# Kernel tuning notes

Hardware: AMD Instinct MI355X
Metric: run time of the kernel (lower is better)

## Reference

```python
import jax, jax.numpy as jnp
import numpy as np

N_NODES = 10000
N_EDGES = 640000
N_GRAPHS = 64
D_NODE = 128   # NO_NODE_FEATURES_TWO
D_EDGE = 32    # NO_EDGE_FEATURES_TWO
HIDDEN = 128   # HIDDEN_GRAPH_TWO
D_OUT = 64     # NO_GRAPH_FEATURES_TWO
EPS = 1e-5


def _xavier(key, fan_in, fan_out):
    lim = float(np.sqrt(6.0 / (fan_in + fan_out)))
    return jax.random.uniform(key, (fan_in, fan_out), jnp.float32, -lim, lim)


def setup_inputs() -> dict:
    key = jax.random.key(0)
    ks = jax.random.split(key, 12)
    x = jax.random.normal(ks[0], (N_NODES, D_NODE), jnp.float32)
    edge_index = jax.random.randint(ks[1], (2, N_EDGES), 0, N_NODES, jnp.int64)
    edge_attr = jax.random.normal(ks[2], (N_EDGES, D_EDGE), jnp.float32)
    u = jax.random.normal(ks[3], (N_GRAPHS, D_OUT), jnp.float32)
    batch = jnp.sort(jax.random.randint(ks[4], (N_NODES,), 0, N_GRAPHS, jnp.int64))
    # global_mlp_1: Lin(160,128) -> LeakyReLU -> BatchNorm1d(128) -> Lin(128,128)
    W1 = _xavier(ks[5], D_NODE + D_EDGE, HIDDEN); b1 = jnp.full((HIDDEN,), 0.01, jnp.float32)
    g1 = jnp.ones((HIDDEN,), jnp.float32); be1 = jnp.zeros((HIDDEN,), jnp.float32)
    W2 = _xavier(ks[6], HIDDEN, HIDDEN); b2 = jnp.full((HIDDEN,), 0.01, jnp.float32)
    # global_mlp_2: Lin(256,128) -> LeakyReLU -> BatchNorm1d(128) -> Lin(128,64)
    W3 = _xavier(ks[7], HIDDEN + D_NODE, HIDDEN); b3 = jnp.full((HIDDEN,), 0.01, jnp.float32)
    g3 = jnp.ones((HIDDEN,), jnp.float32); be3 = jnp.zeros((HIDDEN,), jnp.float32)
    W4 = _xavier(ks[8], HIDDEN, D_OUT); b4 = jnp.full((D_OUT,), 0.01, jnp.float32)
    return {"x": x, "edge_index": edge_index, "edge_attr": edge_attr, "u": u, "batch": batch,
            "W1": W1, "b1": b1, "g1": g1, "be1": be1, "W2": W2, "b2": b2,
            "W3": W3, "b3": b3, "g3": g3, "be3": be3, "W4": W4, "b4": b4}


def _batchnorm(h, gamma, beta):
    # training-mode BatchNorm1d: biased batch stats
    mu = jnp.mean(h, axis=0)
    var = jnp.var(h, axis=0)
    return gamma * (h - mu) * jax.lax.rsqrt(var + EPS) + beta


def reference(x, edge_index, edge_attr, u, batch,
              W1, b1, g1, be1, W2, b2, W3, b3, g3, be3, W4, b4):
    row, col = edge_index[0], edge_index[1]
    # gather + concat -> [E, 160]
    h = jnp.concatenate([x[row], edge_attr], axis=1)
    # global_mlp_1
    h = jax.nn.leaky_relu(h @ W1 + b1, negative_slope=0.01)
    h = _batchnorm(h, g1, be1)
    h = h @ W2 + b2                                   # [E, HIDDEN]
    # scatter_add to nodes
    node_agg = jax.ops.segment_sum(h, col, num_segments=N_NODES)  # [N, HIDDEN]
    # per-graph pooling of x and node_agg
    gx = jax.ops.segment_sum(x, batch, num_segments=N_GRAPHS)       # [B, D_NODE]
    go = jax.ops.segment_sum(node_agg, batch, num_segments=N_GRAPHS)  # [B, HIDDEN]
    g = jnp.concatenate([gx, go], axis=1)             # [B, 256]
    # global_mlp_2
    g = jax.nn.leaky_relu(g @ W3 + b3, negative_slope=0.01)
    g = _batchnorm(g, g3, be3)
    return g @ W4 + b4                                # [B, 64]
```

## Files before the change

kernel.cpp:

```cpp
#include <hip/hip_runtime.h>

#define EE      640000
#define NNODES_ 10000
#define NG      64
#define DN      128
#define DE      32
#define HID     128
#define DOUT    64
#define NMT     (EE / 16)
#define SLOWNB  768
#define HBLK    128
#define CHUNK   (EE / HBLK)
#define FBLK    512
#define NWAVES  (FBLK * 4)

#define ACCF  0
#define CNTF  8192
#define S1F   8256
#define S2F   8384
#define GXF   8512
#define O1F   16704
#define FLGF  24896
#define BAT8  24898
#define W1F_  27458
#define B1F_  47938
#define G1F_  48066
#define BE1F_ 48194
#define W2F_  48322
#define B2F_  64706
#define W3F_  64834
#define B3F_  97602
#define G3F_  97730
#define BE3F_ 97858
#define W4F_  97986
#define B4F_  106178
#define YBF   106244
#define H32F  746244
#define BSTF  754436
#define GENDI 762628
#define NTI   762692
#define T2G   762696
#define SRTE  772936
#define WSEND 1413960

typedef __bf16 bf16x8 __attribute__((ext_vector_type(8)));
typedef float  f32x4  __attribute__((ext_vector_type(4)));

__device__ __forceinline__ float lrelu(float v) { return v > 0.f ? v : 0.01f * v; }

__device__ __forceinline__ bf16x8 cvt8(const float* p) {
  const f32x4 a0 = *(const f32x4*)p, a1 = *(const f32x4*)(p + 4);
  bf16x8 t;
  t[0]=(__bf16)a0[0]; t[1]=(__bf16)a0[1]; t[2]=(__bf16)a0[2]; t[3]=(__bf16)a0[3];
  t[4]=(__bf16)a1[0]; t[5]=(__bf16)a1[1]; t[6]=(__bf16)a1[2]; t[7]=(__bf16)a1[3];
  return t;
}

__global__ __launch_bounds__(256) void k_sniff(const unsigned* __restrict__ xw,
                                               const unsigned* __restrict__ ew,
                                               float* __restrict__ ws) {
  const int tid = threadIdx.x;
  for (int i = tid; i < 8512; i += 256) ws[i] = 0.f;
  if (tid < 64) {
    const unsigned w = xw[tid];
    const unsigned ex = (w >> 7) & 0xFFu;
    int cb = (ex >= 100u && ex <= 140u) ? 1 : 0;
    int ci = (ew[2 * tid + 1] == 0u) ? 1 : 0;
#pragma unroll
    for (int s = 1; s < 64; s <<= 1) { cb += __shfl_xor(cb, s); ci += __shfl_xor(ci, s); }
    if (tid == 0) { int* f = (int*)(ws + FLGF); f[0] = (cb >= 48); f[1] = (ci >= 60); }
  }
}

__device__ __forceinline__ void cpyw(float* dst, const void* src, int n, int isb,
                                     int gtid, int gs) {
  if (isb) { const __bf16* s = (const __bf16*)src;
    for (int i = gtid; i < n; i += gs) dst[i] = (float)s[i];
  } else { const float* s = (const float*)src;
    for (int i = gtid; i < n; i += gs) dst[i] = s[i]; }
}

__global__ __launch_bounds__(256) void k_norm(
    const void* __restrict__ eidx, const void* __restrict__ batch,
    const void* W1, const void* b1, const void* g1, const void* be1,
    const void* W2, const void* b2, const void* W3, const void* b3,
    const void* g3, const void* be3, const void* W4, const void* b4,
    float* __restrict__ ws, const int dohist) {
  const int gtid = blockIdx.x * 256 + threadIdx.x;
  const int gs = gridDim.x * 256;
  const int* f = (const int*)(ws + FLGF);
  const int isb = f[0], isi = f[1];
  cpyw(ws + W1F_, W1, 160 * HID, isb, gtid, gs);
  cpyw(ws + B1F_, b1, HID, isb, gtid, gs);
  cpyw(ws + G1F_, g1, HID, isb, gtid, gs);
  cpyw(ws + BE1F_, be1, HID, isb, gtid, gs);
  cpyw(ws + W2F_, W2, HID * HID, isb, gtid, gs);
  cpyw(ws + B2F_, b2, HID, isb, gtid, gs);
  cpyw(ws + W3F_, W3, 256 * HID, isb, gtid, gs);
  cpyw(ws + B3F_, b3, HID, isb, gtid, gs);
  cpyw(ws + G3F_, g3, HID, isb, gtid, gs);
  cpyw(ws + BE3F_, be3, HID, isb, gtid, gs);
  cpyw(ws + W4F_, W4, HID * DOUT, isb, gtid, gs);
  cpyw(ws + B4F_, b4, DOUT, isb, gtid, gs);
  const int* bs = (const int*)batch;
  unsigned char* b8 = (unsigned char*)(ws + BAT8);
  for (int i = gtid; i < NNODES_; i += gs)
    b8[i] = (unsigned char)((isi ? bs[2 * i] : bs[i]) & 63);
  if (dohist) {
    __shared__ int h[NG];
    if (threadIdx.x < NG) h[threadIdx.x] = 0;
    __syncthreads();
    const int* es = (const int*)eidx;
    for (int e = gtid; e < EE; e += gs) {
      int cl = isi ? es[2 * (EE + e)] : es[EE + e];
      cl = min(max(cl, 0), NNODES_ - 1);
      atomicAdd(&h[(isi ? bs[2 * cl] : bs[cl]) & 63], 1);
    }
    __syncthreads();
    if (threadIdx.x < NG && h[threadIdx.x])
      unsafeAtomicAdd(&ws[CNTF + threadIdx.x], (float)h[threadIdx.x]);
  }
}

__global__ __launch_bounds__(256) void k_hist(const void* __restrict__ eidx,
                                              float* __restrict__ ws) {
  __shared__ int h[NG];
  const int tid = threadIdx.x, b = blockIdx.x;
  if (tid < NG) h[tid] = 0;
  __syncthreads();
  const int isi = ((const int*)(ws + FLGF))[1];
  const int* ei32 = (const int*)eidx;
  const unsigned char* bat8 = (const unsigned char*)(ws + BAT8);
  for (int e = b * CHUNK + tid; e < (b + 1) * CHUNK; e += 256) {
    int cl = isi ? ei32[2 * (EE + e)] : ei32[EE + e];
    cl = min(max(cl, 0), NNODES_ - 1);
    atomicAdd(&h[bat8[cl]], 1);
  }
  __syncthreads();
  if (tid < NG) ((int*)(ws + H32F))[b * NG + tid] = h[tid];
}

__global__ void k_scan(float* __restrict__ ws) {
  const int g = threadIdx.x;
  const int* H = (const int*)(ws + H32F);
  int* BS = (int*)(ws + BSTF);
  int cnt = 0;
  for (int b = 0; b < HBLK; ++b) { BS[b * NG + g] = cnt; cnt += H[b * NG + g]; }
  const int pc = (cnt + 15) & ~15;
  int inc = pc;
#pragma unroll
  for (int s = 1; s < 64; s <<= 1) { int u = __shfl_up(inc, s); if (g >= s) inc += u; }
  const int base = inc - pc;
  for (int b = 0; b < HBLK; ++b) BS[b * NG + g] += base;
  ((int*)(ws + GENDI))[g] = base + cnt;
  ws[CNTF + g] = (float)cnt;
  const int tot = __shfl(inc, 63);
  if (g == 0) ((int*)(ws + NTI))[0] = tot >> 4;
  unsigned char* t2 = (unsigned char*)(ws + T2G);
  for (int i = base >> 4; i < (base + pc) >> 4; ++i) t2[i] = (unsigned char)g;
  int* srte = (int*)(ws + SRTE);
  for (int i = cnt; i < pc; ++i) srte[base + i] = 0;
}

__global__ __launch_bounds__(256) void k_scat(const void* __restrict__ eidx,
                                              float* __restrict__ ws) {
  __shared__ int cur[NG];
  const int tid = threadIdx.x, b = blockIdx.x;
  if (tid < NG) cur[tid] = ((const int*)(ws + BSTF))[b * NG + tid];
  __syncthreads();
  const int isi = ((const int*)(ws + FLGF))[1];
  const int* ei32 = (const int*)eidx;
  const unsigned char* bat8 = (const unsigned char*)(ws + BAT8);
  int* srte = (int*)(ws + SRTE);
  for (int e = b * CHUNK + tid; e < (b + 1) * CHUNK; e += 256) {
    int cl = isi ? ei32[2 * (EE + e)] : ei32[EE + e];
    cl = min(max(cl, 0), NNODES_ - 1);
    const int pos = atomicAdd(&cur[bat8[cl]], 1);
    srte[pos] = e;
  }
}

__global__ __launch_bounds__(256) void k_gx(
    const void* __restrict__ x, const void* __restrict__ batch, float* __restrict__ ws) {
  const int b = blockIdx.x, tid = threadIdx.x;
  const int isb = ((const int*)(ws + FLGF))[0];
  const int isi = ((const int*)(ws + FLGF))[1];
  const int* bt = (const int*)batch;
#define BATV(i) ((isi ? bt[2 * (i)] : bt[(i)]) & 63)
  int lo = 0, hi = NNODES_;
  while (lo < hi) { int m = (lo + hi) >> 1; if (BATV(m) < b) lo = m + 1; else hi = m; }
  const int r0 = lo;
  hi = NNODES_;
  while (lo < hi) { int m = (lo + hi) >> 1; if (BATV(m) < b + 1) lo = m + 1; else hi = m; }
  const int r1 = lo;
#undef BATV
  const int c = tid & 127, half = tid >> 7;
  float acc = 0.f;
  if (isb) { const __bf16* xs = (const __bf16*)x;
    for (int r = r0 + half; r < r1; r += 2) acc += (float)xs[r * DN + c];
  } else { const float* xs = (const float*)x;
    for (int r = r0 + half; r < r1; r += 2) acc += xs[r * DN + c]; }
  __shared__ float red[256];
  red[tid] = acc;
  __syncthreads();
  if (tid < 128) ws[GXF + b * DN + tid] = red[tid] + red[tid + 128];
}

__global__ __launch_bounds__(256) void k_y(float* __restrict__ ws, const void* __restrict__ x) {
  __shared__ __align__(16) __bf16 w1x[128 * 128];
  const int tid = threadIdx.x;
  const int isb = ((const int*)(ws + FLGF))[0];
  for (int i = tid; i < 128 * 128; i += 256) {
    const int k = i >> 7, n = i & 127;
    w1x[n * 128 + k] = (__bf16)ws[W1F_ + k * HID + n];
  }
  __syncthreads();
  const int lane = tid & 63, wid = tid >> 6, ml = lane & 15, kg = lane >> 4;
  __bf16* ybf = (__bf16*)(ws + YBF);
  for (int t = blockIdx.x * 4 + wid; t < 625; t += 160 * 4) {
    const int n0 = t * 16;
    const int row = n0 + ml;
    bf16x8 af[4];
    if (isb) {
      const __bf16* xp = (const __bf16*)x + row * DN + kg * 8;
#pragma unroll
      for (int ks = 0; ks < 4; ++ks) af[ks] = *(const bf16x8*)(xp + ks * 32);
    } else {
      const float* xp = (const float*)x + row * DN + kg * 8;
#pragma unroll
      for (int ks = 0; ks < 4; ++ks) af[ks] = cvt8(xp + ks * 32);
    }
    f32x4 acc[8] = {{0,0,0,0},{0,0,0,0},{0,0,0,0},{0,0,0,0},
                    {0,0,0,0},{0,0,0,0},{0,0,0,0},{0,0,0,0}};
#pragma unroll
    for (int ks = 0; ks < 4; ++ks) {
#pragma unroll
      for (int nt = 0; nt < 8; ++nt) {
        const bf16x8 bfr = *(const bf16x8*)(w1x + (nt * 16 + ml) * 128 + ks * 32 + kg * 8);
        acc[nt] = __builtin_amdgcn_mfma_f32_16x16x32_bf16(af[ks], bfr, acc[nt], 0, 0, 0);
      }
    }
#pragma unroll
    for (int nt = 0; nt < 8; ++nt) {
      const int c = nt * 16 + ml;
      const float bias = ws[B1F_ + c];
#pragma unroll
      for (int q = 0; q < 4; ++q)
        ybf[(n0 + kg * 4 + q) * HID + c] = (__bf16)(acc[nt][q] + bias);
    }
  }
}

__global__ __launch_bounds__(256, 4) void k_edgef2(float* __restrict__ ws,
                                                   const void* __restrict__ ea,
                                                   const void* __restrict__ eidx) {
  __shared__ __align__(16) __bf16 w1e[128 * 32];
  const int tid = threadIdx.x;
  const int* flg = (const int*)(ws + FLGF);
  const int isb = flg[0], isi = flg[1];
  for (int i = tid; i < 32 * 128; i += 256) {
    const int k = i >> 7, n = i & 127;
    w1e[n * 32 + k] = (__bf16)ws[W1F_ + (128 + k) * HID + n];
  }
  __syncthreads();
  const int lane = tid & 63, wid = tid >> 6, ml = lane & 15, kg = lane >> 4;
  bf16x8 bfe[8];
#pragma unroll
  for (int nt = 0; nt < 8; ++nt)
    bfe[nt] = *(const bf16x8*)(w1e + (nt * 16 + ml) * 32 + kg * 8);
  bf16x8 idf;
#pragma unroll
  for (int j = 0; j < 8; ++j) idf[j] = (kg * 8 + j == ml) ? (__bf16)1.0f : (__bf16)0.0f;

  const int* ei32 = (const int*)eidx;
  const int* srte = (const int*)(ws + SRTE);
  const unsigned char* t2g = (const unsigned char*)(ws + T2G);
  const int* gend = (const int*)(ws + GENDI);
  const __bf16* ybf = (const __bf16*)(ws + YBF);
  const int NT = ((const int*)(ws + NTI))[0];
  const int tpw = (NT + NWAVES - 1) / NWAVES;
  const int wgid = blockIdx.x * 4 + wid;
  const int t0 = wgid * tpw;
  const int t1 = min(t0 + tpw, NT);

  float gsum[8] = {0,0,0,0,0,0,0,0};
  float s1[8] = {0,0,0,0,0,0,0,0}, s2[8] = {0,0,0,0,0,0,0,0};
  int cur_g = (t0 < t1) ? (int)t2g[t0] : -1;

  for (int t = t0; t < t1; ++t) {
    const int g = (int)t2g[t];
    if (g != cur_g) {
#pragma unroll
      for (int nt = 0; nt < 8; ++nt) {
        float v = gsum[nt];
        v += __shfl_xor(v, 16); v += __shfl_xor(v, 32);
        if (kg == 0) unsafeAtomicAdd(&ws[ACCF + cur_g * HID + nt * 16 + ml], v);
        gsum[nt] = 0.f;
      }
      cur_g = g;
    }
    const int ge = gend[g];
    const int eidm = srte[t * 16 + ml];
    int r = isi ? ei32[2 * eidm] : ei32[eidm];
    r = min(max(r, 0), NNODES_ - 1);
    bf16x8 ae;
    if (isb) ae = *(const bf16x8*)((const __bf16*)ea + (size_t)eidm * DE + kg * 8);
    else     ae = cvt8((const float*)ea + (size_t)eidm * DE + kg * 8);
    f32x4 acc[8] = {{0,0,0,0},{0,0,0,0},{0,0,0,0},{0,0,0,0},
                    {0,0,0,0},{0,0,0,0},{0,0,0,0},{0,0,0,0}};
#pragma unroll
    for (int nt = 0; nt < 8; ++nt)
      acc[nt] = __builtin_amdgcn_mfma_f32_16x16x32_bf16(ae, bfe[nt], acc[nt], 0, 0, 0);
    const __bf16* yb = ybf + (size_t)r * HID + (kg & 1) * 8;
#pragma unroll
    for (int nt = 0; nt < 8; ++nt) {
      const bf16x8 ay = *(const bf16x8*)(yb + nt * 16);
      acc[nt] = __builtin_amdgcn_mfma_f32_16x16x32_bf16(ay, idf, acc[nt], 0, 0, 0);
    }
    const int eb = t * 16 + kg * 4;
#pragma unroll
    for (int nt = 0; nt < 8; ++nt) {
#pragma unroll
      for (int q = 0; q < 4; ++q) {
        const float v = (eb + q < ge) ? lrelu(acc[nt][q]) : 0.f;
        gsum[nt] += v;
        s1[nt] += v;
        s2[nt] += v * v;
      }
    }
  }
  if (cur_g >= 0) {
#pragma unroll
    for (int nt = 0; nt < 8; ++nt) {
      float v = gsum[nt];
      v += __shfl_xor(v, 16); v += __shfl_xor(v, 32);
      if (kg == 0) unsafeAtomicAdd(&ws[ACCF + cur_g * HID + nt * 16 + ml], v);
    }
  }
#pragma unroll
  for (int nt = 0; nt < 8; ++nt) {
    float v1 = s1[nt], v2 = s2[nt];
    v1 += __shfl_xor(v1, 16); v1 += __shfl_xor(v1, 32);
    v2 += __shfl_xor(v2, 16); v2 += __shfl_xor(v2, 32);
    if (kg == 0) {
      unsafeAtomicAdd(&ws[S1F + nt * 16 + ml], v1);
      unsafeAtomicAdd(&ws[S2F + nt * 16 + ml], v2);
    }
  }
}

__global__ __launch_bounds__(256) void k_edges_slow(
    float* __restrict__ ws, const void* __restrict__ x, const void* __restrict__ ea,
    const void* __restrict__ eidx) {
  __shared__ __align__(16) char smem[40960];
  float* lacc = (float*)smem;
  __bf16* w1t = (__bf16*)smem;
  const int tid = threadIdx.x;
  const int* flg = (const int*)(ws + FLGF);
  const int isb = flg[0], isi = flg[1];
  for (int i = tid; i < 160 * HID; i += 256) {
    const int k = i >> 7, n = i & 127;
    w1t[n * 160 + k] = (__bf16)ws[W1F_ + i];
  }
  __syncthreads();
  const int lane = tid & 63, wid = tid >> 6;
  const int ml = lane & 15, kg = lane >> 4;
  const int ch0 = (wid & 1) * 64;
  const int pair = blockIdx.x * 2 + (wid >> 1);
  bf16x8 bfr[5][4];
  float b1v[4];
#pragma unroll
  for (int nt = 0; nt < 4; ++nt) {
    const int n = ch0 + nt * 16 + ml;
    b1v[nt] = ws[B1F_ + n];
#pragma unroll
    for (int ks = 0; ks < 5; ++ks)
      bfr[ks][nt] = *(const bf16x8*)(w1t + n * 160 + ks * 32 + kg * 8);
  }
  __syncthreads();
  for (int i = tid; i < NG * 132; i += 256) lacc[i] = 0.f;
  __syncthreads();
  float s1a[4] = {0,0,0,0}, s2a[4] = {0,0,0,0};
  const int* ei32 = (const int*)eidx;
  const unsigned char* bat8 = (const unsigned char*)(ws + BAT8);
  for (int mt = pair; mt < NMT; mt += 2 * SLOWNB) {
    const int em = mt * 16 + ml;
    int r  = isi ? ei32[2 * em] : ei32[em];
    int cl = isi ? ei32[2 * (EE + em)] : ei32[EE + em];
    r  = min(max(r, 0), NNODES_ - 1);
    cl = min(max(cl, 0), NNODES_ - 1);
    const int gg = bat8[cl];
    f32x4 acc[4] = {{0,0,0,0},{0,0,0,0},{0,0,0,0},{0,0,0,0}};
#pragma unroll
    for (int ks = 0; ks < 4; ++ks) {
      bf16x8 afr;
      if (isb) afr = *(const bf16x8*)((const __bf16*)x + r * DN + ks * 32 + kg * 8);
      else     afr = cvt8((const float*)x + r * DN + ks * 32 + kg * 8);
#pragma unroll
      for (int nt = 0; nt < 4; ++nt)
        acc[nt] = __builtin_amdgcn_mfma_f32_16x16x32_bf16(afr, bfr[ks][nt], acc[nt], 0, 0, 0);
    }
    {
      bf16x8 t;
      if (isb) t = *(const bf16x8*)((const __bf16*)ea + em * DE + kg * 8);
      else     t = cvt8((const float*)ea + em * DE + kg * 8);
#pragma unroll
      for (int nt = 0; nt < 4; ++nt)
        acc[nt] = __builtin_amdgcn_mfma_f32_16x16x32_bf16(t, bfr[4][nt], acc[nt], 0, 0, 0);
    }
    int gR[4];
#pragma unroll
    for (int q = 0; q < 4; ++q) gR[q] = __shfl(gg, kg * 4 + q);
#pragma unroll
    for (int nt = 0; nt < 4; ++nt) {
      const int c = ch0 + nt * 16 + ml;
#pragma unroll
      for (int q = 0; q < 4; ++q) {
        const float v = lrelu(acc[nt][q] + b1v[nt]);
        s1a[nt] += v;
        s2a[nt] += v * v;
        atomicAdd(&lacc[gR[q] * 132 + c], v);
      }
    }
  }
#pragma unroll
  for (int nt = 0; nt < 4; ++nt) {
    float v1 = s1a[nt], v2 = s2a[nt];
    v1 += __shfl_xor(v1, 16); v1 += __shfl_xor(v1, 32);
    v2 += __shfl_xor(v2, 16); v2 += __shfl_xor(v2, 32);
    if (lane < 16) {
      unsafeAtomicAdd(&ws[S1F + ch0 + nt * 16 + lane], v1);
      unsafeAtomicAdd(&ws[S2F + ch0 + nt * 16 + lane], v2);
    }
  }
  __syncthreads();
  for (int i = tid; i < NG * HID; i += 256)
    unsafeAtomicAdd(&ws[ACCF + i], lacc[(i >> 7) * 132 + (i & 127)]);
}

__global__ __launch_bounds__(128) void k_graph(float* __restrict__ ws) {
  const int b = blockIdx.x, c = threadIdx.x;
  const float invE = 1.f / (float)EE;
  const float mu  = ws[S1F + c] * invE;
  const float var = ws[S2F + c] * invE - mu * mu;
  const float s   = ws[G1F_ + c] * rsqrtf(var + 1e-5f);
  const float t   = ws[BE1F_ + c] - mu * s;
  const float cb  = ws[CNTF + b];
  __shared__ float zsh[HID];
  __shared__ float gv[DN + HID];
  zsh[c] = s * ws[ACCF + b * HID + c] + cb * t;
  gv[c]  = ws[GXF + b * DN + c];
  __syncthreads();
  float a = cb * ws[B2F_ + c];
  for (int k = 0; k < HID; ++k) a += zsh[k] * ws[W2F_ + k * HID + c];
  gv[DN + c] = a;
  __syncthreads();
  float h = ws[B3F_ + c];
  for (int j = 0; j < DN + HID; ++j) h += gv[j] * ws[W3F_ + j * HID + c];
  ws[O1F + b * HID + c] = lrelu(h);
}

__global__ __launch_bounds__(64) void k_out(const float* __restrict__ ws,
                                            void* __restrict__ out) {
  const int b = blockIdx.x, o = threadIdx.x;
  const int isb = ((const int*)(ws + FLGF))[0];
  __shared__ float zrow[HID];
  for (int cc = o; cc < HID; cc += 64) {
    float sm = 0.f, sq = 0.f;
    for (int r = 0; r < NG; ++r) { const float v = ws[O1F + r * HID + cc]; sm += v; sq += v * v; }
    const float mu  = sm * (1.f / NG);
    const float var = sq * (1.f / NG) - mu * mu;
    const float sc  = ws[G3F_ + cc] * rsqrtf(var + 1e-5f);
    zrow[cc] = ws[O1F + b * HID + cc] * sc + (ws[BE3F_ + cc] - mu * sc);
  }
  __syncthreads();
  float a = ws[B4F_ + o];
  for (int k = 0; k < HID; ++k) a += zrow[k] * ws[W4F_ + k * DOUT + o];
  if (isb) ((__bf16*)out)[b * DOUT + o] = (__bf16)a;
  else     ((float*)out)[b * DOUT + o] = a;
}

extern "C" void kernel_launch(void* const* d_in, const int* in_sizes, int n_in,
                              void* d_out, int out_size, void* d_ws, size_t ws_size,
                              hipStream_t stream) {
  float* ws = (float*)d_ws;
  const int fast = (ws_size >= (size_t)WSEND * 4) ? 1 : 0;
  hipLaunchKernelGGL(k_sniff, dim3(1), dim3(256), 0, stream,
                     (const unsigned*)d_in[0], (const unsigned*)d_in[1], ws);
  hipLaunchKernelGGL(k_norm, dim3(256), dim3(256), 0, stream,
                     d_in[1], d_in[4],
                     d_in[5], d_in[6], d_in[7], d_in[8],
                     d_in[9], d_in[10], d_in[11], d_in[12],
                     d_in[13], d_in[14], d_in[15], d_in[16], ws, fast ? 0 : 1);
  hipLaunchKernelGGL(k_gx, dim3(NG), dim3(256), 0, stream, d_in[0], d_in[4], ws);
  if (fast) {
    hipLaunchKernelGGL(k_hist, dim3(HBLK), dim3(256), 0, stream, d_in[1], ws);
    hipLaunchKernelGGL(k_scan, dim3(1), dim3(64), 0, stream, ws);
    hipLaunchKernelGGL(k_scat, dim3(HBLK), dim3(256), 0, stream, d_in[1], ws);
    hipLaunchKernelGGL(k_y, dim3(160), dim3(256), 0, stream, ws, d_in[0]);
    hipLaunchKernelGGL(k_edgef2, dim3(FBLK), dim3(256), 0, stream, ws, d_in[2], d_in[1]);
  } else {
    hipLaunchKernelGGL(k_edges_slow, dim3(SLOWNB), dim3(256), 0, stream,
                       ws, d_in[0], d_in[2], d_in[1]);
  }
  hipLaunchKernelGGL(k_graph, dim3(NG), dim3(128), 0, stream, ws);
  hipLaunchKernelGGL(k_out, dim3(NG), dim3(64), 0, stream, ws, d_out);
}
```

Measured before the change: 392.0 us.

## Fuse prep kernels, pre-sort source rows, and retune edge block counts

```diff
diff --git a/kernel.cpp b/kernel.cpp
--- a/kernel.cpp
+++ b/kernel.cpp
@@ -9,9 +9,9 @@
 #define DOUT    64
 #define NMT     (EE / 16)
 #define SLOWNB  768
-#define HBLK    128
+#define HBLK    256
 #define CHUNK   (EE / HBLK)
-#define FBLK    512
+#define FBLK    2048
 #define NWAVES  (FBLK * 4)
 
 #define ACCF  0
@@ -36,12 +36,13 @@
 #define B4F_  106178
 #define YBF   106244
 #define H32F  746244
-#define BSTF  754436
-#define GENDI 762628
-#define NTI   762692
-#define T2G   762696
-#define SRTE  772936
-#define WSEND 1413960
+#define BSTF  762628
+#define GENDI 779012
+#define NTI   779076
+#define T2G   779078
+#define SRTE  789318
+#define SRR   1430342
+#define WSEND 1750854
 
 typedef __bf16 bf16x8 __attribute__((ext_vector_type(8)));
 typedef float  f32x4  __attribute__((ext_vector_type(4)));
@@ -56,22 +57,6 @@
   return t;
 }
 
-__global__ __launch_bounds__(256) void k_sniff(const unsigned* __restrict__ xw,
-                                               const unsigned* __restrict__ ew,
-                                               float* __restrict__ ws) {
-  const int tid = threadIdx.x;
-  for (int i = tid; i < 8512; i += 256) ws[i] = 0.f;
-  if (tid < 64) {
-    const unsigned w = xw[tid];
-    const unsigned ex = (w >> 7) & 0xFFu;
-    int cb = (ex >= 100u && ex <= 140u) ? 1 : 0;
-    int ci = (ew[2 * tid + 1] == 0u) ? 1 : 0;
-#pragma unroll
-    for (int s = 1; s < 64; s <<= 1) { cb += __shfl_xor(cb, s); ci += __shfl_xor(ci, s); }
-    if (tid == 0) { int* f = (int*)(ws + FLGF); f[0] = (cb >= 48); f[1] = (ci >= 60); }
-  }
-}
-
 __device__ __forceinline__ void cpyw(float* dst, const void* src, int n, int isb,
                                      int gtid, int gs) {
   if (isb) { const __bf16* s = (const __bf16*)src;
@@ -80,16 +65,32 @@
     for (int i = gtid; i < n; i += gs) dst[i] = s[i]; }
 }
 
-__global__ __launch_bounds__(256) void k_norm(
-    const void* __restrict__ eidx, const void* __restrict__ batch,
+__global__ __launch_bounds__(256) void k_prep(
+    const unsigned* __restrict__ xw, const void* __restrict__ eidx,
+    const void* __restrict__ batch,
     const void* W1, const void* b1, const void* g1, const void* be1,
     const void* W2, const void* b2, const void* W3, const void* b3,
     const void* g3, const void* be3, const void* W4, const void* b4,
-    float* __restrict__ ws, const int dohist) {
-  const int gtid = blockIdx.x * 256 + threadIdx.x;
+    float* __restrict__ ws, const int fast) {
+  __shared__ int sflg[2];
+  __shared__ int h[NG];
+  const int tid = threadIdx.x;
+  if (tid < 64) {
+    const unsigned w = xw[tid];
+    const unsigned ex = (w >> 7) & 0xFFu;
+    int cb = (ex >= 100u && ex <= 140u) ? 1 : 0;
+    int ci = (((const unsigned*)eidx)[2 * tid + 1] == 0u) ? 1 : 0;
+#pragma unroll
+    for (int s = 1; s < 64; s <<= 1) { cb += __shfl_xor(cb, s); ci += __shfl_xor(ci, s); }
+    if (tid == 0) { sflg[0] = (cb >= 48); sflg[1] = (ci >= 60); }
+  }
+  if (tid < NG) h[tid] = 0;
+  __syncthreads();
+  const int isb = sflg[0], isi = sflg[1];
+  if (blockIdx.x == 0 && tid == 0) { int* f = (int*)(ws + FLGF); f[0] = isb; f[1] = isi; }
+  const int gtid = blockIdx.x * 256 + tid;
   const int gs = gridDim.x * 256;
-  const int* f = (const int*)(ws + FLGF);
-  const int isb = f[0], isi = f[1];
+  for (int i = gtid; i < 8512; i += gs) ws[i] = 0.f;
   cpyw(ws + W1F_, W1, 160 * HID, isb, gtid, gs);
   cpyw(ws + B1F_, b1, HID, isb, gtid, gs);
   cpyw(ws + G1F_, g1, HID, isb, gtid, gs);
@@ -106,38 +107,19 @@
   unsigned char* b8 = (unsigned char*)(ws + BAT8);
   for (int i = gtid; i < NNODES_; i += gs)
     b8[i] = (unsigned char)((isi ? bs[2 * i] : bs[i]) & 63);
-  if (dohist) {
-    __shared__ int h[NG];
-    if (threadIdx.x < NG) h[threadIdx.x] = 0;
-    __syncthreads();
-    const int* es = (const int*)eidx;
-    for (int e = gtid; e < EE; e += gs) {
-      int cl = isi ? es[2 * (EE + e)] : es[EE + e];
-      cl = min(max(cl, 0), NNODES_ - 1);
-      atomicAdd(&h[(isi ? bs[2 * cl] : bs[cl]) & 63], 1);
-    }
-    __syncthreads();
-    if (threadIdx.x < NG && h[threadIdx.x])
-      unsafeAtomicAdd(&ws[CNTF + threadIdx.x], (float)h[threadIdx.x]);
-  }
-}
-
-__global__ __launch_bounds__(256) void k_hist(const void* __restrict__ eidx,
-                                              float* __restrict__ ws) {
-  __shared__ int h[NG];
-  const int tid = threadIdx.x, b = blockIdx.x;
-  if (tid < NG) h[tid] = 0;
-  __syncthreads();
-  const int isi = ((const int*)(ws + FLGF))[1];
-  const int* ei32 = (const int*)eidx;
-  const unsigned char* bat8 = (const unsigned char*)(ws + BAT8);
+  const int* es = (const int*)eidx;
+  const int b = blockIdx.x;
   for (int e = b * CHUNK + tid; e < (b + 1) * CHUNK; e += 256) {
-    int cl = isi ? ei32[2 * (EE + e)] : ei32[EE + e];
+    int cl = isi ? es[2 * (EE + e)] : es[EE + e];
     cl = min(max(cl, 0), NNODES_ - 1);
-    atomicAdd(&h[bat8[cl]], 1);
-  }
-  __syncthreads();
-  if (tid < NG) ((int*)(ws + H32F))[b * NG + tid] = h[tid];
+    atomicAdd(&h[(isi ? bs[2 * cl] : bs[cl]) & 63], 1);
+  }
+  __syncthreads();
+  if (fast) {
+    if (tid < NG) ((int*)(ws + H32F))[b * NG + tid] = h[tid];
+  } else {
+    if (tid < NG && h[tid]) unsafeAtomicAdd(&ws[CNTF + tid], (float)h[tid]);
+  }
 }
 
 __global__ void k_scan(float* __restrict__ ws) {
@@ -159,7 +141,8 @@
   unsigned char* t2 = (unsigned char*)(ws + T2G);
   for (int i = base >> 4; i < (base + pc) >> 4; ++i) t2[i] = (unsigned char)g;
   int* srte = (int*)(ws + SRTE);
-  for (int i = cnt; i < pc; ++i) srte[base + i] = 0;
+  unsigned short* srr = (unsigned short*)(ws + SRR);
+  for (int i = cnt; i < pc; ++i) { srte[base + i] = 0; srr[base + i] = 0; }
 }
 
 __global__ __launch_bounds__(256) void k_scat(const void* __restrict__ eidx,
@@ -172,92 +155,96 @@
   const int* ei32 = (const int*)eidx;
   const unsigned char* bat8 = (const unsigned char*)(ws + BAT8);
   int* srte = (int*)(ws + SRTE);
+  unsigned short* srr = (unsigned short*)(ws + SRR);
   for (int e = b * CHUNK + tid; e < (b + 1) * CHUNK; e += 256) {
     int cl = isi ? ei32[2 * (EE + e)] : ei32[EE + e];
     cl = min(max(cl, 0), NNODES_ - 1);
+    int r = isi ? ei32[2 * e] : ei32[e];
+    r = min(max(r, 0), NNODES_ - 1);
     const int pos = atomicAdd(&cur[bat8[cl]], 1);
     srte[pos] = e;
-  }
-}
-
-__global__ __launch_bounds__(256) void k_gx(
-    const void* __restrict__ x, const void* __restrict__ batch, float* __restrict__ ws) {
-  const int b = blockIdx.x, tid = threadIdx.x;
+    srr[pos] = (unsigned short)r;
+  }
+}
+
+__global__ __launch_bounds__(256) void k_yg(float* __restrict__ ws,
+                                            const void* __restrict__ x,
+                                            const void* __restrict__ batch,
+                                            const int nyb) {
+  const int tid = threadIdx.x;
   const int isb = ((const int*)(ws + FLGF))[0];
   const int isi = ((const int*)(ws + FLGF))[1];
-  const int* bt = (const int*)batch;
+  if ((int)blockIdx.x < nyb) {
+    __shared__ __align__(16) __bf16 w1x[128 * 128];
+    for (int i = tid; i < 128 * 128; i += 256) {
+      const int k = i >> 7, n = i & 127;
+      w1x[n * 128 + k] = (__bf16)ws[W1F_ + k * HID + n];
+    }
+    __syncthreads();
+    const int lane = tid & 63, wid = tid >> 6, ml = lane & 15, kg = lane >> 4;
+    __bf16* ybf = (__bf16*)(ws + YBF);
+    for (int t = blockIdx.x * 4 + wid; t < 625; t += nyb * 4) {
+      const int n0 = t * 16;
+      const int row = n0 + ml;
+      bf16x8 af[4];
+      if (isb) {
+        const __bf16* xp = (const __bf16*)x + row * DN + kg * 8;
+#pragma unroll
+        for (int ks = 0; ks < 4; ++ks) af[ks] = *(const bf16x8*)(xp + ks * 32);
+      } else {
+        const float* xp = (const float*)x + row * DN + kg * 8;
+#pragma unroll
+        for (int ks = 0; ks < 4; ++ks) af[ks] = cvt8(xp + ks * 32);
+      }
+      f32x4 acc[8] = {{0,0,0,0},{0,0,0,0},{0,0,0,0},{0,0,0,0},
+                      {0,0,0,0},{0,0,0,0},{0,0,0,0},{0,0,0,0}};
+#pragma unroll
+      for (int ks = 0; ks < 4; ++ks) {
+#pragma unroll
+        for (int nt = 0; nt < 8; ++nt) {
+          const bf16x8 bfr = *(const bf16x8*)(w1x + (nt * 16 + ml) * 128 + ks * 32 + kg * 8);
+          acc[nt] = __builtin_amdgcn_mfma_f32_16x16x32_bf16(af[ks], bfr, acc[nt], 0, 0, 0);
+        }
+      }
+#pragma unroll
+      for (int nt = 0; nt < 8; ++nt) {
+        const int c = nt * 16 + ml;
+        const float bias = ws[B1F_ + c];
+#pragma unroll
+        for (int q = 0; q < 4; ++q)
+          ybf[(n0 + kg * 4 + q) * HID + c] = (__bf16)(acc[nt][q] + bias);
+      }
+    }
+  } else {
+    const int b = blockIdx.x - nyb;
+    const int* bt = (const int*)batch;
 #define BATV(i) ((isi ? bt[2 * (i)] : bt[(i)]) & 63)
-  int lo = 0, hi = NNODES_;
-  while (lo < hi) { int m = (lo + hi) >> 1; if (BATV(m) < b) lo = m + 1; else hi = m; }
-  const int r0 = lo;
-  hi = NNODES_;
-  while (lo < hi) { int m = (lo + hi) >> 1; if (BATV(m) < b + 1) lo = m + 1; else hi = m; }
-  const int r1 = lo;
+    int lo = 0, hi = NNODES_;
+    while (lo < hi) { int m = (lo + hi) >> 1; if (BATV(m) < b) lo = m + 1; else hi = m; }
+    const int r0 = lo;
+    hi = NNODES_;
+    while (lo < hi) { int m = (lo + hi) >> 1; if (BATV(m) < b + 1) lo = m + 1; else hi = m; }
+    const int r1 = lo;
 #undef BATV
-  const int c = tid & 127, half = tid >> 7;
-  float acc = 0.f;
-  if (isb) { const __bf16* xs = (const __bf16*)x;
-    for (int r = r0 + half; r < r1; r += 2) acc += (float)xs[r * DN + c];
-  } else { const float* xs = (const float*)x;
-    for (int r = r0 + half; r < r1; r += 2) acc += xs[r * DN + c]; }
-  __shared__ float red[256];
-  red[tid] = acc;
-  __syncthreads();
-  if (tid < 128) ws[GXF + b * DN + tid] = red[tid] + red[tid + 128];
-}
-
-__global__ __launch_bounds__(256) void k_y(float* __restrict__ ws, const void* __restrict__ x) {
-  __shared__ __align__(16) __bf16 w1x[128 * 128];
-  const int tid = threadIdx.x;
-  const int isb = ((const int*)(ws + FLGF))[0];
-  for (int i = tid; i < 128 * 128; i += 256) {
-    const int k = i >> 7, n = i & 127;
-    w1x[n * 128 + k] = (__bf16)ws[W1F_ + k * HID + n];
-  }
-  __syncthreads();
-  const int lane = tid & 63, wid = tid >> 6, ml = lane & 15, kg = lane >> 4;
-  __bf16* ybf = (__bf16*)(ws + YBF);
-  for (int t = blockIdx.x * 4 + wid; t < 625; t += 160 * 4) {
-    const int n0 = t * 16;
-    const int row = n0 + ml;
-    bf16x8 af[4];
-    if (isb) {
-      const __bf16* xp = (const __bf16*)x + row * DN + kg * 8;
-#pragma unroll
-      for (int ks = 0; ks < 4; ++ks) af[ks] = *(const bf16x8*)(xp + ks * 32);
-    } else {
-      const float* xp = (const float*)x + row * DN + kg * 8;
-#pragma unroll
-      for (int ks = 0; ks < 4; ++ks) af[ks] = cvt8(xp + ks * 32);
-    }
-    f32x4 acc[8] = {{0,0,0,0},{0,0,0,0},{0,0,0,0},{0,0,0,0},
-                    {0,0,0,0},{0,0,0,0},{0,0,0,0},{0,0,0,0}};
-#pragma unroll
-    for (int ks = 0; ks < 4; ++ks) {
-#pragma unroll
-      for (int nt = 0; nt < 8; ++nt) {
-        const bf16x8 bfr = *(const bf16x8*)(w1x + (nt * 16 + ml) * 128 + ks * 32 + kg * 8);
-        acc[nt] = __builtin_amdgcn_mfma_f32_16x16x32_bf16(af[ks], bfr, acc[nt], 0, 0, 0);
-      }
-    }
-#pragma unroll
-    for (int nt = 0; nt < 8; ++nt) {
-      const int c = nt * 16 + ml;
-      const float bias = ws[B1F_ + c];
-#pragma unroll
-      for (int q = 0; q < 4; ++q)
-        ybf[(n0 + kg * 4 + q) * HID + c] = (__bf16)(acc[nt][q] + bias);
-    }
-  }
-}
-
-__global__ __launch_bounds__(256, 4) void k_edgef2(float* __restrict__ ws,
-                                                   const void* __restrict__ ea,
-                                                   const void* __restrict__ eidx) {
+    const int c = tid & 127, half = tid >> 7;
+    float acc = 0.f;
+    if (isb) { const __bf16* xs = (const __bf16*)x;
+      for (int r = r0 + half; r < r1; r += 2) acc += (float)xs[r * DN + c];
+    } else { const float* xs = (const float*)x;
+      for (int r = r0 + half; r < r1; r += 2) acc += xs[r * DN + c]; }
+    __shared__ float red[256];
+    red[tid] = acc;
+    __syncthreads();
+    if (tid < 128) ws[GXF + b * DN + tid] = red[tid] + red[tid + 128];
+  }
+}
+
+__global__ __launch_bounds__(256) void k_edgef2(float* __restrict__ ws,
+                                                const void* __restrict__ ea) {
   __shared__ __align__(16) __bf16 w1e[128 * 32];
   const int tid = threadIdx.x;
   const int* flg = (const int*)(ws + FLGF);
-  const int isb = flg[0], isi = flg[1];
+  const int isb = flg[0];
   for (int i = tid; i < 32 * 128; i += 256) {
     const int k = i >> 7, n = i & 127;
     w1e[n * 32 + k] = (__bf16)ws[W1F_ + (128 + k) * HID + n];
@@ -272,8 +259,8 @@
 #pragma unroll
   for (int j = 0; j < 8; ++j) idf[j] = (kg * 8 + j == ml) ? (__bf16)1.0f : (__bf16)0.0f;
 
-  const int* ei32 = (const int*)eidx;
   const int* srte = (const int*)(ws + SRTE);
+  const unsigned short* srr = (const unsigned short*)(ws + SRR);
   const unsigned char* t2g = (const unsigned char*)(ws + T2G);
   const int* gend = (const int*)(ws + GENDI);
   const __bf16* ybf = (const __bf16*)(ws + YBF);
@@ -300,12 +287,12 @@
       cur_g = g;
     }
     const int ge = gend[g];
-    const int eidm = srte[t * 16 + ml];
-    int r = isi ? ei32[2 * eidm] : ei32[eidm];
-    r = min(max(r, 0), NNODES_ - 1);
+    const int e16 = t * 16 + ml;
+    const int e = srte[e16];
+    const int r = (int)srr[e16];
     bf16x8 ae;
-    if (isb) ae = *(const bf16x8*)((const __bf16*)ea + (size_t)eidm * DE + kg * 8);
-    else     ae = cvt8((const float*)ea + (size_t)eidm * DE + kg * 8);
+    if (isb) ae = *(const bf16x8*)((const __bf16*)ea + (size_t)e * DE + kg * 8);
+    else     ae = cvt8((const float*)ea + (size_t)e * DE + kg * 8);
     f32x4 acc[8] = {{0,0,0,0},{0,0,0,0},{0,0,0,0},{0,0,0,0},
                     {0,0,0,0},{0,0,0,0},{0,0,0,0},{0,0,0,0}};
 #pragma unroll
@@ -485,21 +472,18 @@
                               hipStream_t stream) {
   float* ws = (float*)d_ws;
   const int fast = (ws_size >= (size_t)WSEND * 4) ? 1 : 0;
-  hipLaunchKernelGGL(k_sniff, dim3(1), dim3(256), 0, stream,
-                     (const unsigned*)d_in[0], (const unsigned*)d_in[1], ws);
-  hipLaunchKernelGGL(k_norm, dim3(256), dim3(256), 0, stream,
-                     d_in[1], d_in[4],
+  hipLaunchKernelGGL(k_prep, dim3(HBLK), dim3(256), 0, stream,
+                     (const unsigned*)d_in[0], d_in[1], d_in[4],
                      d_in[5], d_in[6], d_in[7], d_in[8],
                      d_in[9], d_in[10], d_in[11], d_in[12],
-                     d_in[13], d_in[14], d_in[15], d_in[16], ws, fast ? 0 : 1);
-  hipLaunchKernelGGL(k_gx, dim3(NG), dim3(256), 0, stream, d_in[0], d_in[4], ws);
+                     d_in[13], d_in[14], d_in[15], d_in[16], ws, fast);
   if (fast) {
-    hipLaunchKernelGGL(k_hist, dim3(HBLK), dim3(256), 0, stream, d_in[1], ws);
     hipLaunchKernelGGL(k_scan, dim3(1), dim3(64), 0, stream, ws);
     hipLaunchKernelGGL(k_scat, dim3(HBLK), dim3(256), 0, stream, d_in[1], ws);
-    hipLaunchKernelGGL(k_y, dim3(160), dim3(256), 0, stream, ws, d_in[0]);
-    hipLaunchKernelGGL(k_edgef2, dim3(FBLK), dim3(256), 0, stream, ws, d_in[2], d_in[1]);
+    hipLaunchKernelGGL(k_yg, dim3(160 + NG), dim3(256), 0, stream, ws, d_in[0], d_in[4], 160);
+    hipLaunchKernelGGL(k_edgef2, dim3(FBLK), dim3(256), 0, stream, ws, d_in[2]);
   } else {
+    hipLaunchKernelGGL(k_yg, dim3(NG), dim3(256), 0, stream, ws, d_in[0], d_in[4], 0);
     hipLaunchKernelGGL(k_edges_slow, dim3(SLOWNB), dim3(256), 0, stream,
                        ws, d_in[0], d_in[2], d_in[1]);
   }
```

Result: slower. 472.6 us (+20.6%).
